# Optimization experiments

Measured on AMD Instinct MI355X. Metric: run time of the kernel, lower is better.

The kernel has to match this reference:

```python
import jax, jax.numpy as jnp
import numpy as np

N_NODES = 100000
N_EDGES = 1600000
IN_SIZE, HID_SIZE, OUT_SIZE = 128, 64, 64


def _glorot(key, shape):
    lim = float(np.sqrt(6.0 / (shape[0] + shape[1])))
    return jax.random.uniform(key, shape, jnp.float32, -lim, lim)


def setup_inputs() -> dict:
    key = jax.random.key(0)
    ks = jax.random.split(key, 6)
    features = jax.random.normal(ks[0], (N_NODES, IN_SIZE), jnp.float32)
    src = jax.random.randint(ks[1], (N_EDGES,), 0, N_NODES)
    dst = jax.random.randint(ks[2], (N_EDGES,), 0, N_NODES)
    return {
        "features": features,
        "W0": _glorot(ks[3], (IN_SIZE, HID_SIZE)),
        "b0": jnp.zeros((HID_SIZE,), jnp.float32),
        "W1": _glorot(ks[4], (HID_SIZE, HID_SIZE)),
        "b1": jnp.zeros((HID_SIZE,), jnp.float32),
        "W2": _glorot(ks[5], (HID_SIZE, OUT_SIZE)),
        "b2": jnp.zeros((OUT_SIZE,), jnp.float32),
        "src": src,
        "dst": dst,
    }


def reference(features, W0, b0, W1, b1, W2, b2, src, dst):
    # DGL GraphConv with norm='both': h' = relu(D_in^{-1/2} A D_out^{-1/2} h W + b)
    # Dropout layers are identity in eval mode (deterministic baseline).
    N = features.shape[0]
    ones = jnp.ones(src.shape, features.dtype)
    deg_out = jax.ops.segment_sum(ones, src, num_segments=N)
    deg_in = jax.ops.segment_sum(ones, dst, num_segments=N)
    norm_src = jnp.where(deg_out > 0, deg_out, 1.0) ** -0.5  # [N]
    norm_dst = jnp.where(deg_in > 0, deg_in, 1.0) ** -0.5    # [N]

    def layer(h, W, b):
        h = h * norm_src[:, None]          # source-side degree norm
        m = (h @ W)[src]                   # project first (in >= out), then gather [E, d_out]
        agg = jax.ops.segment_sum(m, dst, num_segments=N)  # scatter-add to destinations
        return jax.nn.relu(agg * norm_dst[:, None] + b)

    h = layer(features, W0, b0)
    h = layer(h, W1, b1)
    return layer(h, W2, b2)
```

## Files before the change

kernel.cpp:

```cpp
#include <hip/hip_runtime.h>
#include <hip/hip_bf16.h>

typedef __hip_bfloat16 bf16;
typedef __attribute__((ext_vector_type(8))) short bf16x8;
typedef __attribute__((ext_vector_type(8))) unsigned short u16x8;
typedef __attribute__((ext_vector_type(4))) float f32x4;
typedef __attribute__((ext_vector_type(4))) int i32x4;
typedef __attribute__((ext_vector_type(4))) short s16x4;

__device__ __forceinline__ float b2f(unsigned short u) {
  return __uint_as_float(((unsigned)u) << 16);
}
__device__ __forceinline__ unsigned short f2b(float x) {
  bf16 h = __float2bfloat16(x);
  return *reinterpret_cast<unsigned short*>(&h);
}

__global__ void k_passA(const int* __restrict__ src, const int* __restrict__ dst, int E,
                        int nbuck, int M, int* __restrict__ counts,
                        const unsigned short* __restrict__ raw, int* __restrict__ flag) {
  if (blockIdx.x == 256) {
    __shared__ int sbad, snz;
    const int t = threadIdx.x;
    if (t == 0) { sbad = 0; snz = 0; }
    __syncthreads();
    const unsigned short u = raw[t];
    const float a = fabsf(b2f(u));
    if (!(a < 100.f)) atomicAdd(&sbad, 1);
    if (((t & 1) == 0) && u != 0) atomicAdd(&snz, 1);
    __syncthreads();
    if (t == 0) flag[0] = (sbad == 0 && snz > 0) ? 1 : 0;
    return;
  }
  extern __shared__ int lh[];
  int* lh1 = lh;
  int* lh2 = lh + nbuck;
  const int t = threadIdx.x;
  for (int k = t; k < 2 * nbuck; k += 256) lh[k] = 0;
  __syncthreads();
  const int chunk = (E + 255) / 256;
  const int s = blockIdx.x * chunk;
  const int e = min(E, s + chunk);
  for (int i = s + t; i < e; i += 256) {
    atomicAdd(&lh1[dst[i] >> 8], 1);
    atomicAdd(&lh2[src[i] >> 8], 1);
  }
  __syncthreads();
  for (int k = t; k < nbuck; k += 256) {
    counts[k * 256 + blockIdx.x] = lh1[k];
    counts[M + k * 256 + blockIdx.x] = lh2[k];
  }
}

__global__ void k_scan1(const int* __restrict__ a, int M2, int* __restrict__ bsums) {
  __shared__ int sdata[256];
  int i = blockIdx.x * 256 + threadIdx.x;
  int v = (i < M2) ? a[i] : 0;
  sdata[threadIdx.x] = v;
  __syncthreads();
  for (int s = 128; s > 0; s >>= 1) {
    if (threadIdx.x < s) sdata[threadIdx.x] += sdata[threadIdx.x + s];
    __syncthreads();
  }
  if (threadIdx.x == 0) bsums[blockIdx.x] = sdata[0];
}

__global__ void k_scan2(int* __restrict__ bsums, int nb, int* __restrict__ rowStart,
                        int N, int E) {
  __shared__ int s[1024];
  const int t = threadIdx.x;
  const int v = (t < nb) ? bsums[t] : 0;
  s[t] = v;
  __syncthreads();
  for (int off = 1; off < 1024; off <<= 1) {
    int u = (t >= off) ? s[t - off] : 0;
    __syncthreads();
    s[t] += u;
    __syncthreads();
  }
  if (t < nb) bsums[t] = s[t] - v;
  if (t == 0) rowStart[N] = E;
}

__global__ void k_scan3(int* __restrict__ a, int M2, const int* __restrict__ bsums) {
  __shared__ int sdata[256];
  int i = blockIdx.x * 256 + threadIdx.x;
  int v = (i < M2) ? a[i] : 0;
  sdata[threadIdx.x] = v;
  __syncthreads();
  for (int off = 1; off < 256; off <<= 1) {
    int t = (threadIdx.x >= off) ? sdata[threadIdx.x - off] : 0;
    __syncthreads();
    sdata[threadIdx.x] += t;
    __syncthreads();
  }
  if (i < M2) a[i] = bsums[blockIdx.x] + sdata[threadIdx.x] - v;
}

__global__ void k_passC(const int* __restrict__ src, const int* __restrict__ dst, int E,
                        int nbuck, int M, const int* __restrict__ S,
                        int* __restrict__ tmp, unsigned char* __restrict__ tmp2) {
  extern __shared__ int cur[];
  int* cur1 = cur;
  int* cur2 = cur + nbuck;
  const int t = threadIdx.x;
  for (int k = t; k < nbuck; k += 256) {
    cur1[k] = S[k * 256 + blockIdx.x];
    cur2[k] = S[M + k * 256 + blockIdx.x];
  }
  __syncthreads();
  const int chunk = (E + 255) / 256;
  const int s = blockIdx.x * chunk;
  const int e = min(E, s + chunk);
  for (int i = s + t; i < e; i += 256) {
    const int sv = src[i];
    const int d = dst[i];
    const int pos1 = atomicAdd(&cur1[d >> 8], 1);
    tmp[pos1] = sv | ((d & 255) << 20);
    const int pos2 = atomicAdd(&cur2[sv >> 8], 1);
    tmp2[pos2 - E] = (unsigned char)(sv & 255);
  }
}

__global__ void k_passD(const int* __restrict__ tmp, const unsigned char* __restrict__ tmp2,
                        const int* __restrict__ S, int nbuck, int M, int N, int E,
                        int* __restrict__ rowStart, int* __restrict__ edgeSrc,
                        float* __restrict__ ns, float* __restrict__ nd) {
  __shared__ int h[256];
  __shared__ int ex[256];
  __shared__ int c[256];
  const int t = threadIdx.x;
  const int k = blockIdx.x;
  const int node = k * 256 + t;
  const int bs2 = S[M + k * 256] - E;
  const int be2 = (k + 1 < nbuck) ? (S[M + (k + 1) * 256] - E) : E;
  h[t] = 0;
  __syncthreads();
  for (int i = bs2 + t; i < be2; i += 256) atomicAdd(&h[tmp2[i]], 1);
  __syncthreads();
  if (node < N) {
    int dov = h[t];
    if (dov <= 0) dov = 1;
    ns[node] = rsqrtf((float)dov);
  }
  __syncthreads();
  const int bs = S[k * 256];
  const int be = (k + 1 < nbuck) ? S[(k + 1) * 256] : E;
  h[t] = 0;
  __syncthreads();
  for (int i = bs + t; i < be; i += 256) atomicAdd(&h[tmp[i] >> 20], 1);
  __syncthreads();
  const int cnt = h[t];
  ex[t] = cnt;
  __syncthreads();
  for (int off = 1; off < 256; off <<= 1) {
    int u = (t >= off) ? ex[t - off] : 0;
    __syncthreads();
    ex[t] += u;
    __syncthreads();
  }
  const int excl = ex[t] - cnt;
  if (node < N) {
    rowStart[node] = bs + excl;
    nd[node] = rsqrtf((float)(cnt > 0 ? cnt : 1));
  }
  c[t] = bs + excl;
  __syncthreads();
  for (int i = bs + t; i < be; i += 256) {
    const int v = tmp[i];
    const int pos = atomicAdd(&c[v >> 20], 1);
    edgeSrc[pos] = v & 0xFFFFF;
  }
}

__global__ void k_prepW(const void* __restrict__ W0, const void* __restrict__ W1,
                        const void* __restrict__ W2, const int* __restrict__ flag,
                        unsigned short* __restrict__ WT0, unsigned short* __restrict__ WT1,
                        unsigned short* __restrict__ WT2) {
  const bool isb = (*flag != 0);
  const int i = blockIdx.x * 256 + threadIdx.x;
  if (i < 8192) {
    const int n = i >> 7, k = i & 127;
    const float v = isb ? b2f(((const unsigned short*)W0)[k * 64 + n])
                        : ((const float*)W0)[k * 64 + n];
    WT0[i] = f2b(v);
  } else if (i < 12288) {
    const int j = i - 8192;
    const int n = j >> 6, k = j & 63;
    const float v = isb ? b2f(((const unsigned short*)W1)[k * 64 + n])
                        : ((const float*)W1)[k * 64 + n];
    WT1[j] = f2b(v);
  } else if (i < 16384) {
    const int j = i - 12288;
    const int n = j >> 6, k = j & 63;
    const float v = isb ? b2f(((const unsigned short*)W2)[k * 64 + n])
                        : ((const float*)W2)[k * 64 + n];
    WT2[j] = f2b(v);
  }
}

template <int K, bool FIRST, bool SCALE>
__device__ __forceinline__ void gemm_loadA(const void* hin, bool isb, int rowA,
                                           int quad, bf16x8* A) {
  constexpr int KT = K / 32;
  if (FIRST && !isb) {
    const float* hp = (const float*)hin + (size_t)rowA * K;
#pragma unroll
    for (int kt = 0; kt < KT; ++kt) {
      const float4 u0 = *(const float4*)(hp + kt * 32 + quad * 8);
      const float4 u1 = *(const float4*)(hp + kt * 32 + quad * 8 + 4);
      A[kt][0] = (short)f2b(u0.x); A[kt][1] = (short)f2b(u0.y);
      A[kt][2] = (short)f2b(u0.z); A[kt][3] = (short)f2b(u0.w);
      A[kt][4] = (short)f2b(u1.x); A[kt][5] = (short)f2b(u1.y);
      A[kt][6] = (short)f2b(u1.z); A[kt][7] = (short)f2b(u1.w);
    }
  } else {
    const unsigned short* hp = (const unsigned short*)hin + (size_t)rowA * K;
#pragma unroll
    for (int kt = 0; kt < KT; ++kt)
      A[kt] = *(const bf16x8*)(hp + kt * 32 + quad * 8);
  }
}

template <int K, bool FIRST, bool SCALE>
__global__ void __launch_bounds__(256) k_gemm(
    const void* __restrict__ hin, const unsigned short* __restrict__ WT,
    const int* __restrict__ flag, const float* __restrict__ norm_src,
    int N, unsigned short* __restrict__ out) {
  constexpr int KT = K / 32;
  constexpr int CST = 72;
  __shared__ unsigned short Cl[4][16 * CST];
  const bool isb = (*flag != 0);
  const int tid = threadIdx.x;
  const int lane = tid & 63;
  const int quad = lane >> 4;
  const int l16 = lane & 15;
  const int w = tid >> 6;
  unsigned short* myC = &Cl[w][0];

  bf16x8 Bf[KT][4];
#pragma unroll
  for (int kt = 0; kt < KT; ++kt)
#pragma unroll
    for (int nt = 0; nt < 4; ++nt)
      Bf[kt][nt] = *(const bf16x8*)(WT + (size_t)(nt * 16 + l16) * K + kt * 32 + quad * 8);

  const int wid = blockIdx.x * 4 + w;
  const int nw = gridDim.x * 4;
  const int G = (N + 15) >> 4;

  bf16x8 A0[KT], A1[KT];
  if (wid < G) {
    int r0 = (wid << 4) + l16;
    if (r0 >= N) r0 = N - 1;
    gemm_loadA<K, FIRST, SCALE>(hin, isb, r0, quad, A0);
  }
  for (int g = wid; g < G; g += nw) {
    if (g + nw < G) {
      int r1 = ((g + nw) << 4) + l16;
      if (r1 >= N) r1 = N - 1;
      gemm_loadA<K, FIRST, SCALE>(hin, isb, r1, quad, A1);
    }
    f32x4 acc[4] = {{0.f, 0.f, 0.f, 0.f}, {0.f, 0.f, 0.f, 0.f},
                    {0.f, 0.f, 0.f, 0.f}, {0.f, 0.f, 0.f, 0.f}};
#pragma unroll
    for (int kt = 0; kt < KT; ++kt) {
#pragma unroll
      for (int nt = 0; nt < 4; ++nt)
        acc[nt] = __builtin_amdgcn_mfma_f32_16x16x32_bf16(A0[kt], Bf[kt][nt], acc[nt], 0, 0, 0);
    }
    const int rowD = quad * 4;
#pragma unroll
    for (int r = 0; r < 4; ++r) {
      const int nodeW = (g << 4) + rowD + r;
      const float f = (SCALE && nodeW < N) ? norm_src[nodeW] : 1.0f;
#pragma unroll
      for (int nt = 0; nt < 4; ++nt)
        myC[(rowD + r) * CST + nt * 16 + l16] = f2b(SCALE ? acc[nt][r] * f : acc[nt][r]);
    }
    const int row2 = lane >> 2;
    const int c0 = (lane & 3) * 16;
    const int node = (g << 4) + row2;
    if (node < N) {
      const u16x8 v0 = *(const u16x8*)&myC[row2 * CST + c0];
      const u16x8 v1 = *(const u16x8*)&myC[row2 * CST + c0 + 8];
      *(u16x8*)(out + (size_t)node * 64 + c0) = v0;
      *(u16x8*)(out + (size_t)node * 64 + c0 + 8) = v1;
    }
#pragma unroll
    for (int kt = 0; kt < KT; ++kt) A0[kt] = A1[kt];
  }
}

__device__ __forceinline__ void agg_chunk_compute(unsigned trbase, int cb32, int lo,
                                                  unsigned span, int quad, f32x4* acc) {
  const int posbase = cb32 + (quad << 2);
  const unsigned u0 = (unsigned)(posbase - lo);
  bf16x8 Af;
#pragma unroll
  for (int j = 0; j < 8; ++j) {
    const unsigned off = (j < 4) ? (unsigned)j : (unsigned)(12 + j);
    Af[j] = ((u0 + off) < span) ? (short)0x3F80 : (short)0;
  }
  s16x4 t0[4], t1[4];
#pragma unroll
  for (int nt = 0; nt < 4; ++nt) {
    const unsigned a = trbase + (unsigned)(nt * 1024);
    asm volatile("ds_read_b64_tr_b16 %0, %1" : "=v"(t0[nt]) : "v"(a) : "memory");
    asm volatile("ds_read_b64_tr_b16 %0, %1 offset:512" : "=v"(t1[nt]) : "v"(a) : "memory");
  }
  asm volatile("s_waitcnt lgkmcnt(0)" ::: "memory");
  __builtin_amdgcn_sched_barrier(0);
#pragma unroll
  for (int nt = 0; nt < 4; ++nt) {
    bf16x8 Bf;
    Bf[0] = t0[nt][0]; Bf[1] = t0[nt][1]; Bf[2] = t0[nt][2]; Bf[3] = t0[nt][3];
    Bf[4] = t1[nt][0]; Bf[5] = t1[nt][1]; Bf[6] = t1[nt][2]; Bf[7] = t1[nt][3];
    acc[nt] = __builtin_amdgcn_mfma_f32_16x16x32_bf16(Af, Bf, acc[nt], 0, 0, 0);
  }
}

template <bool LAST>
__global__ void __launch_bounds__(256) k_aggregate(
    const unsigned short* __restrict__ proj,
    const int* __restrict__ edgeSrc, const int* __restrict__ rowStart,
    const float* __restrict__ norm_dst, const float* __restrict__ norm_src,
    const void* __restrict__ bias, const int* __restrict__ flag,
    int N, int E, void* __restrict__ outp) {
  __shared__ unsigned short lds[4][2048];
  const bool isb = (*flag != 0);
  const int tid = threadIdx.x;
  const int w = tid >> 6;
  const int lane = tid & 63;
  const int l16 = lane & 15;
  const int quad = lane >> 4;
  const int e32 = lane & 31;
  const int p = lane >> 5;

  const int wid = blockIdx.x * 4 + w;
  const int g0 = wid * 8;

  float bcol[4];
#pragma unroll
  for (int nt = 0; nt < 4; ++nt) {
    const int col = nt * 16 + l16;
    bcol[nt] = isb ? b2f(((const unsigned short*)bias)[col]) : ((const float*)bias)[col];
  }

  const int cb = rowStart[min(g0, N)];
  const int ce = rowStart[min(g0 + 8, N)];
  const int L = ce - cb;
  const int nch = (L + 31) >> 5;

  const int rsi = min(g0 + min(l16, 8), N);
  const int rsj = min(g0 + min(l16 + 1, 8), N);
  const int lo = rowStart[rsi];
  const unsigned span = (unsigned)(rowStart[rsj] - lo);

  int idxc[6];
#pragma unroll
  for (int t = 0; t < 6; ++t) {
    const int pos = min(cb + t * 32 + e32, E - 1);
    idxc[t] = edgeSrc[pos];
  }

  unsigned short* myl = &lds[w][0];
  unsigned wofs[4];
#pragma unroll
  for (int q = 0; q < 4; ++q) {
    const int n0 = p * 32 + q * 8;
    wofs[q] = (unsigned)((n0 >> 4) * 512 + e32 * 16 + (n0 & 15));
  }
  const unsigned trbase = (unsigned)(uintptr_t)myl + (unsigned)lane * 8u;

  f32x4 acc[4] = {{0.f, 0.f, 0.f, 0.f}, {0.f, 0.f, 0.f, 0.f},
                  {0.f, 0.f, 0.f, 0.f}, {0.f, 0.f, 0.f, 0.f}};

  i32x4 gb[4][4];
#define AGG_ISSUE(t, b)                                                         \
  {                                                                             \
    const unsigned short* rp = proj + (size_t)idxc[t] * 64 + p * 32;            \
    gb[b][0] = *(const i32x4*)(rp);                                             \
    gb[b][1] = *(const i32x4*)(rp + 8);                                         \
    gb[b][2] = *(const i32x4*)(rp + 16);                                        \
    gb[b][3] = *(const i32x4*)(rp + 24);                                        \
  }
  if (0 < nch) AGG_ISSUE(0, 0);
  if (1 < nch) AGG_ISSUE(1, 1);
  if (2 < nch) AGG_ISSUE(2, 2);
  if (3 < nch) AGG_ISSUE(3, 3);

#pragma unroll
  for (int tt = 0; tt < 6; ++tt) {
    if (tt < nch) {
#pragma unroll
      for (int q = 0; q < 4; ++q) *(i32x4*)(myl + wofs[q]) = gb[tt & 3][q];
      if (tt + 4 < 6 && tt + 4 < nch) AGG_ISSUE(tt + 4, tt & 3);
      asm volatile("s_waitcnt lgkmcnt(0)" ::: "memory");
      agg_chunk_compute(trbase, cb + tt * 32, lo, span, quad, acc);
    }
  }
  for (int t = 6; t < nch; ++t) {
    const int pos = min(cb + t * 32 + e32, E - 1);
    const int idx = edgeSrc[pos];
    const unsigned short* rp = proj + (size_t)idx * 64 + p * 32;
    i32x4 g4[4];
    g4[0] = *(const i32x4*)(rp);
    g4[1] = *(const i32x4*)(rp + 8);
    g4[2] = *(const i32x4*)(rp + 16);
    g4[3] = *(const i32x4*)(rp + 24);
#pragma unroll
    for (int q = 0; q < 4; ++q) *(i32x4*)(myl + wofs[q]) = g4[q];
    asm volatile("s_waitcnt lgkmcnt(0)" ::: "memory");
    agg_chunk_compute(trbase, cb + t * 32, lo, span, quad, acc);
  }
#undef AGG_ISSUE

  if (LAST && !isb) {
    float* fs = (float*)myl;
#pragma unroll
    for (int reg = 0; reg < 4; ++reg) {
      const int row = quad * 4 + reg;
      if (row < 8) {
        const int node = min(g0 + row, N - 1);
        const float nd = norm_dst[node];
#pragma unroll
        for (int nt = 0; nt < 4; ++nt)
          fs[row * 64 + nt * 16 + l16] = fmaxf(fmaf(acc[nt][reg], nd, bcol[nt]), 0.f);
      }
    }
    asm volatile("s_waitcnt lgkmcnt(0)" ::: "memory");
    __builtin_amdgcn_sched_barrier(0);
    const int r = lane >> 3;
    const int c0 = (lane & 7) * 8;
    const int node = g0 + r;
    if (node < N) {
      const float4 v0 = *(const float4*)&fs[r * 64 + c0];
      const float4 v1 = *(const float4*)&fs[r * 64 + c0 + 4];
      float* of = (float*)outp + (size_t)node * 64 + c0;
      *(float4*)of = v0;
      *(float4*)(of + 4) = v1;
    }
  } else {
#pragma unroll
    for (int reg = 0; reg < 4; ++reg) {
      const int row = quad * 4 + reg;
      if (row < 8) {
        const int node = min(g0 + row, N - 1);
        const float nd = norm_dst[node];
        const float esc = LAST ? 1.f : norm_src[node];
#pragma unroll
        for (int nt = 0; nt < 4; ++nt) {
          float x = fmaxf(fmaf(acc[nt][reg], nd, bcol[nt]), 0.f);
          if (!LAST) x *= esc;
          myl[row * 64 + nt * 16 + l16] = f2b(x);
        }
      }
    }
    asm volatile("s_waitcnt lgkmcnt(0)" ::: "memory");
    __builtin_amdgcn_sched_barrier(0);
    if (lane < 32) {
      const int r = lane >> 2;
      const int c0 = (lane & 3) * 16;
      const int node = g0 + r;
      if (node < N) {
        const u16x8 v0 = *(const u16x8*)&myl[r * 64 + c0];
        const u16x8 v1 = *(const u16x8*)&myl[r * 64 + c0 + 8];
        *(u16x8*)((unsigned short*)outp + (size_t)node * 64 + c0) = v0;
        *(u16x8*)((unsigned short*)outp + (size_t)node * 64 + c0 + 8) = v1;
      }
    }
  }
}

extern "C" void kernel_launch(void* const* d_in, const int* in_sizes, int n_in,
                              void* d_out, int out_size, void* d_ws, size_t ws_size,
                              hipStream_t stream) {
  const void* features = d_in[0];
  const void* W0 = d_in[1];
  const void* b0 = d_in[2];
  const void* W1 = d_in[3];
  const void* b1 = d_in[4];
  const void* W2 = d_in[5];
  const void* b2 = d_in[6];
  const int* src = (const int*)d_in[7];
  const int* dst = (const int*)d_in[8];
  const int N = in_sizes[0] / 128;
  const int E = in_sizes[7];
  const int NBUCK = (N + 255) >> 8;
  const int M = NBUCK * 256;
  const int M2 = 2 * M;

  char* w = (char*)d_ws;
  size_t off = 0;
  auto alloc = [&](size_t bytes) {
    void* p = w + off;
    off = (off + bytes + 255) & ~(size_t)255;
    return p;
  };
  int* flag = (int*)alloc(4);
  int* rowStart = (int*)alloc((size_t)(N + 1) * 4);
  int* counts = (int*)alloc((size_t)M2 * 4);
  int* bsums = (int*)alloc(1024 * 4);
  float* norm_src = (float*)alloc((size_t)N * 4);
  float* norm_dst = (float*)alloc((size_t)N * 4);
  int* tmp = (int*)alloc((size_t)E * 4);
  unsigned char* tmp2 = (unsigned char*)alloc((size_t)E);
  int* edgeSrc = (int*)alloc((size_t)E * 4);
  unsigned short* projA = (unsigned short*)alloc((size_t)N * 64 * 2);
  unsigned short* WT0 = (unsigned short*)alloc(64 * 128 * 2);
  unsigned short* WT1 = (unsigned short*)alloc(64 * 64 * 2);
  unsigned short* WT2 = (unsigned short*)alloc(64 * 64 * 2);
  unsigned short* hB = (unsigned short*)d_out;

  const size_t lds_nb = (size_t)NBUCK * 2 * 4;
  const int G16 = (N + 15) / 16;
  const int GB = (G16 + 7) / 8;

  k_passA<<<257, 256, lds_nb, stream>>>(src, dst, E, NBUCK, M, counts,
                                        (const unsigned short*)features, flag);
  const int NB2 = (M2 + 255) / 256;
  k_scan1<<<NB2, 256, 0, stream>>>(counts, M2, bsums);
  k_scan2<<<1, 1024, 0, stream>>>(bsums, NB2, rowStart, N, E);
  k_scan3<<<NB2, 256, 0, stream>>>(counts, M2, bsums);
  k_passC<<<256, 256, lds_nb, stream>>>(src, dst, E, NBUCK, M, counts, tmp, tmp2);
  k_passD<<<NBUCK, 256, 0, stream>>>(tmp, tmp2, counts, NBUCK, M, N, E,
                                     rowStart, edgeSrc, norm_src, norm_dst);
  k_prepW<<<64, 256, 0, stream>>>(W0, W1, W2, flag, WT0, WT1, WT2);

  const int AB = (((N + 7) / 8) + 3) / 4;
  k_gemm<128, true, true><<<GB, 256, 0, stream>>>(features, WT0, flag, norm_src, N, projA);
  k_aggregate<false><<<AB, 256, 0, stream>>>(projA, edgeSrc, rowStart, norm_dst, norm_src, b0, flag, N, E, hB);
  k_gemm<64, false, false><<<GB, 256, 0, stream>>>(hB, WT1, flag, nullptr, N, projA);
  k_aggregate<false><<<AB, 256, 0, stream>>>(projA, edgeSrc, rowStart, norm_dst, norm_src, b1, flag, N, E, hB);
  k_gemm<64, false, false><<<GB, 256, 0, stream>>>(hB, WT2, flag, nullptr, N, projA);
  k_aggregate<true><<<AB, 256, 0, stream>>>(projA, edgeSrc, rowStart, norm_dst, norm_src, b2, flag, N, E, d_out);
}
```

Baseline: 335.3 us.

## Use global atomic out-degree, fold weight prep into GEMM, shrink gather prefetch

Out-degree is now counted with global atomics into a memset array rather than through a second bucket histogram, scatter and per-bucket count. This removes the tmp2 byte array, halves the scan size and drops work from passC and passD. The separate weight-transpose kernel is gone: each GEMM block converts and transposes its weight matrix into LDS and reads B fragments from there. The aggregation prefetch depth is reduced from 4 to 2 chunks. The trade-offs are contended global atomics on random source ids, redundant per-block weight loading, and less latency hiding in the gather.

```diff
diff --git a/kernel.cpp b/kernel.cpp
--- a/kernel.cpp
+++ b/kernel.cpp
@@ -17,8 +17,9 @@
 }
 
 __global__ void k_passA(const int* __restrict__ src, const int* __restrict__ dst, int E,
-                        int nbuck, int M, int* __restrict__ counts,
-                        const unsigned short* __restrict__ raw, int* __restrict__ flag) {
+                        int nbuck, int* __restrict__ counts,
+                        const unsigned short* __restrict__ raw, int* __restrict__ flag,
+                        int* __restrict__ degout) {
   if (blockIdx.x == 256) {
     __shared__ int sbad, snz;
     const int t = threadIdx.x;
@@ -32,30 +33,25 @@
     if (t == 0) flag[0] = (sbad == 0 && snz > 0) ? 1 : 0;
     return;
   }
-  extern __shared__ int lh[];
-  int* lh1 = lh;
-  int* lh2 = lh + nbuck;
+  extern __shared__ int lh1[];
   const int t = threadIdx.x;
-  for (int k = t; k < 2 * nbuck; k += 256) lh[k] = 0;
+  for (int k = t; k < nbuck; k += 256) lh1[k] = 0;
   __syncthreads();
   const int chunk = (E + 255) / 256;
   const int s = blockIdx.x * chunk;
   const int e = min(E, s + chunk);
   for (int i = s + t; i < e; i += 256) {
     atomicAdd(&lh1[dst[i] >> 8], 1);
-    atomicAdd(&lh2[src[i] >> 8], 1);
-  }
-  __syncthreads();
-  for (int k = t; k < nbuck; k += 256) {
-    counts[k * 256 + blockIdx.x] = lh1[k];
-    counts[M + k * 256 + blockIdx.x] = lh2[k];
-  }
-}
-
-__global__ void k_scan1(const int* __restrict__ a, int M2, int* __restrict__ bsums) {
+    atomicAdd(&degout[src[i]], 1);
+  }
+  __syncthreads();
+  for (int k = t; k < nbuck; k += 256) counts[k * 256 + blockIdx.x] = lh1[k];
+}
+
+__global__ void k_scan1(const int* __restrict__ a, int M, int* __restrict__ bsums) {
   __shared__ int sdata[256];
   int i = blockIdx.x * 256 + threadIdx.x;
-  int v = (i < M2) ? a[i] : 0;
+  int v = (i < M) ? a[i] : 0;
   sdata[threadIdx.x] = v;
   __syncthreads();
   for (int s = 128; s > 0; s >>= 1) {
@@ -82,10 +78,10 @@
   if (t == 0) rowStart[N] = E;
 }
 
-__global__ void k_scan3(int* __restrict__ a, int M2, const int* __restrict__ bsums) {
+__global__ void k_scan3(int* __restrict__ a, int M, const int* __restrict__ bsums) {
   __shared__ int sdata[256];
   int i = blockIdx.x * 256 + threadIdx.x;
-  int v = (i < M2) ? a[i] : 0;
+  int v = (i < M) ? a[i] : 0;
   sdata[threadIdx.x] = v;
   __syncthreads();
   for (int off = 1; off < 256; off <<= 1) {
@@ -94,20 +90,14 @@
     sdata[threadIdx.x] += t;
     __syncthreads();
   }
-  if (i < M2) a[i] = bsums[blockIdx.x] + sdata[threadIdx.x] - v;
+  if (i < M) a[i] = bsums[blockIdx.x] + sdata[threadIdx.x] - v;
 }
 
 __global__ void k_passC(const int* __restrict__ src, const int* __restrict__ dst, int E,
-                        int nbuck, int M, const int* __restrict__ S,
-                        int* __restrict__ tmp, unsigned char* __restrict__ tmp2) {
-  extern __shared__ int cur[];
-  int* cur1 = cur;
-  int* cur2 = cur + nbuck;
+                        int nbuck, const int* __restrict__ S, int* __restrict__ tmp) {
+  extern __shared__ int cur1[];
   const int t = threadIdx.x;
-  for (int k = t; k < nbuck; k += 256) {
-    cur1[k] = S[k * 256 + blockIdx.x];
-    cur2[k] = S[M + k * 256 + blockIdx.x];
-  }
+  for (int k = t; k < nbuck; k += 256) cur1[k] = S[k * 256 + blockIdx.x];
   __syncthreads();
   const int chunk = (E + 255) / 256;
   const int s = blockIdx.x * chunk;
@@ -117,14 +107,13 @@
     const int d = dst[i];
     const int pos1 = atomicAdd(&cur1[d >> 8], 1);
     tmp[pos1] = sv | ((d & 255) << 20);
-    const int pos2 = atomicAdd(&cur2[sv >> 8], 1);
-    tmp2[pos2 - E] = (unsigned char)(sv & 255);
-  }
-}
-
-__global__ void k_passD(const int* __restrict__ tmp, const unsigned char* __restrict__ tmp2,
-                        const int* __restrict__ S, int nbuck, int M, int N, int E,
+  }
+}
+
+__global__ void k_passD(const int* __restrict__ tmp, const int* __restrict__ S,
+                        int nbuck, int N, int E,
                         int* __restrict__ rowStart, int* __restrict__ edgeSrc,
+                        const int* __restrict__ degout,
                         float* __restrict__ ns, float* __restrict__ nd) {
   __shared__ int h[256];
   __shared__ int ex[256];
@@ -132,18 +121,6 @@
   const int t = threadIdx.x;
   const int k = blockIdx.x;
   const int node = k * 256 + t;
-  const int bs2 = S[M + k * 256] - E;
-  const int be2 = (k + 1 < nbuck) ? (S[M + (k + 1) * 256] - E) : E;
-  h[t] = 0;
-  __syncthreads();
-  for (int i = bs2 + t; i < be2; i += 256) atomicAdd(&h[tmp2[i]], 1);
-  __syncthreads();
-  if (node < N) {
-    int dov = h[t];
-    if (dov <= 0) dov = 1;
-    ns[node] = rsqrtf((float)dov);
-  }
-  __syncthreads();
   const int bs = S[k * 256];
   const int be = (k + 1 < nbuck) ? S[(k + 1) * 256] : E;
   h[t] = 0;
@@ -163,6 +140,9 @@
   if (node < N) {
     rowStart[node] = bs + excl;
     nd[node] = rsqrtf((float)(cnt > 0 ? cnt : 1));
+    int dov = degout[node];
+    if (dov <= 0) dov = 1;
+    ns[node] = rsqrtf((float)dov);
   }
   c[t] = bs + excl;
   __syncthreads();
@@ -170,32 +150,6 @@
     const int v = tmp[i];
     const int pos = atomicAdd(&c[v >> 20], 1);
     edgeSrc[pos] = v & 0xFFFFF;
-  }
-}
-
-__global__ void k_prepW(const void* __restrict__ W0, const void* __restrict__ W1,
-                        const void* __restrict__ W2, const int* __restrict__ flag,
-                        unsigned short* __restrict__ WT0, unsigned short* __restrict__ WT1,
-                        unsigned short* __restrict__ WT2) {
-  const bool isb = (*flag != 0);
-  const int i = blockIdx.x * 256 + threadIdx.x;
-  if (i < 8192) {
-    const int n = i >> 7, k = i & 127;
-    const float v = isb ? b2f(((const unsigned short*)W0)[k * 64 + n])
-                        : ((const float*)W0)[k * 64 + n];
-    WT0[i] = f2b(v);
-  } else if (i < 12288) {
-    const int j = i - 8192;
-    const int n = j >> 6, k = j & 63;
-    const float v = isb ? b2f(((const unsigned short*)W1)[k * 64 + n])
-                        : ((const float*)W1)[k * 64 + n];
-    WT1[j] = f2b(v);
-  } else if (i < 16384) {
-    const int j = i - 12288;
-    const int n = j >> 6, k = j & 63;
-    const float v = isb ? b2f(((const unsigned short*)W2)[k * 64 + n])
-                        : ((const float*)W2)[k * 64 + n];
-    WT2[j] = f2b(v);
   }
 }
 
@@ -224,27 +178,46 @@
 
 template <int K, bool FIRST, bool SCALE>
 __global__ void __launch_bounds__(256) k_gemm(
-    const void* __restrict__ hin, const unsigned short* __restrict__ WT,
+    const void* __restrict__ hin, const void* __restrict__ Wv,
     const int* __restrict__ flag, const float* __restrict__ norm_src,
     int N, unsigned short* __restrict__ out) {
   constexpr int KT = K / 32;
+  constexpr int ST = K + 8;
   constexpr int CST = 72;
+  __shared__ unsigned short Wl[64 * ST];
   __shared__ unsigned short Cl[4][16 * CST];
   const bool isb = (*flag != 0);
   const int tid = threadIdx.x;
+
+  {
+    const unsigned short* Wus = (const unsigned short*)Wv;
+    const float* Wf = (const float*)Wv;
+    for (int i0 = tid * 8; i0 < K * 64; i0 += 2048) {
+      const int k = i0 >> 6;
+      const int n0 = i0 & 63;
+      unsigned short v[8];
+      if (isb) {
+        const u16x8 u = *(const u16x8*)(Wus + i0);
+#pragma unroll
+        for (int j = 0; j < 8; ++j) v[j] = u[j];
+      } else {
+        const float4 f0 = *(const float4*)(Wf + i0);
+        const float4 f1 = *(const float4*)(Wf + i0 + 4);
+        v[0] = f2b(f0.x); v[1] = f2b(f0.y); v[2] = f2b(f0.z); v[3] = f2b(f0.w);
+        v[4] = f2b(f1.x); v[5] = f2b(f1.y); v[6] = f2b(f1.z); v[7] = f2b(f1.w);
+      }
+#pragma unroll
+      for (int j = 0; j < 8; ++j) Wl[(n0 + j) * ST + k] = v[j];
+    }
+  }
+  __syncthreads();
+
   const int lane = tid & 63;
   const int quad = lane >> 4;
   const int l16 = lane & 15;
   const int w = tid >> 6;
   unsigned short* myC = &Cl[w][0];
 
-  bf16x8 Bf[KT][4];
-#pragma unroll
-  for (int kt = 0; kt < KT; ++kt)
-#pragma unroll
-    for (int nt = 0; nt < 4; ++nt)
-      Bf[kt][nt] = *(const bf16x8*)(WT + (size_t)(nt * 16 + l16) * K + kt * 32 + quad * 8);
-
   const int wid = blockIdx.x * 4 + w;
   const int nw = gridDim.x * 4;
   const int G = (N + 15) >> 4;
@@ -265,9 +238,12 @@
                     {0.f, 0.f, 0.f, 0.f}, {0.f, 0.f, 0.f, 0.f}};
 #pragma unroll
     for (int kt = 0; kt < KT; ++kt) {
-#pragma unroll
-      for (int nt = 0; nt < 4; ++nt)
-        acc[nt] = __builtin_amdgcn_mfma_f32_16x16x32_bf16(A0[kt], Bf[kt][nt], acc[nt], 0, 0, 0);
+      const int koff = kt * 32 + quad * 8;
+#pragma unroll
+      for (int nt = 0; nt < 4; ++nt) {
+        const bf16x8 Bf = *(const bf16x8*)&Wl[(nt * 16 + l16) * ST + koff];
+        acc[nt] = __builtin_amdgcn_mfma_f32_16x16x32_bf16(A0[kt], Bf, acc[nt], 0, 0, 0);
+      }
     }
     const int rowD = quad * 4;
 #pragma unroll
@@ -376,7 +352,7 @@
   f32x4 acc[4] = {{0.f, 0.f, 0.f, 0.f}, {0.f, 0.f, 0.f, 0.f},
                   {0.f, 0.f, 0.f, 0.f}, {0.f, 0.f, 0.f, 0.f}};
 
-  i32x4 gb[4][4];
+  i32x4 gb[2][4];
 #define AGG_ISSUE(t, b)                                                         \
   {                                                                             \
     const unsigned short* rp = proj + (size_t)idxc[t] * 64 + p * 32;            \
@@ -387,15 +363,13 @@
   }
   if (0 < nch) AGG_ISSUE(0, 0);
   if (1 < nch) AGG_ISSUE(1, 1);
-  if (2 < nch) AGG_ISSUE(2, 2);
-  if (3 < nch) AGG_ISSUE(3, 3);
 
 #pragma unroll
   for (int tt = 0; tt < 6; ++tt) {
     if (tt < nch) {
 #pragma unroll
-      for (int q = 0; q < 4; ++q) *(i32x4*)(myl + wofs[q]) = gb[tt & 3][q];
-      if (tt + 4 < 6 && tt + 4 < nch) AGG_ISSUE(tt + 4, tt & 3);
+      for (int q = 0; q < 4; ++q) *(i32x4*)(myl + wofs[q]) = gb[tt & 1][q];
+      if (tt + 2 < 6 && tt + 2 < nch) AGG_ISSUE(tt + 2, tt & 1);
       asm volatile("s_waitcnt lgkmcnt(0)" ::: "memory");
       agg_chunk_compute(trbase, cb + tt * 32, lo, span, quad, acc);
     }
@@ -489,7 +463,6 @@
   const int E = in_sizes[7];
   const int NBUCK = (N + 255) >> 8;
   const int M = NBUCK * 256;
-  const int M2 = 2 * M;
 
   char* w = (char*)d_ws;
   size_t off = 0;
@@ -500,39 +473,35 @@
   };
   int* flag = (int*)alloc(4);
   int* rowStart = (int*)alloc((size_t)(N + 1) * 4);
-  int* counts = (int*)alloc((size_t)M2 * 4);
+  int* counts = (int*)alloc((size_t)M * 4);
   int* bsums = (int*)alloc(1024 * 4);
   float* norm_src = (float*)alloc((size_t)N * 4);
   float* norm_dst = (float*)alloc((size_t)N * 4);
+  int* degout = (int*)alloc((size_t)N * 4);
   int* tmp = (int*)alloc((size_t)E * 4);
-  unsigned char* tmp2 = (unsigned char*)alloc((size_t)E);
   int* edgeSrc = (int*)alloc((size_t)E * 4);
   unsigned short* projA = (unsigned short*)alloc((size_t)N * 64 * 2);
-  unsigned short* WT0 = (unsigned short*)alloc(64 * 128 * 2);
-  unsigned short* WT1 = (unsigned short*)alloc(64 * 64 * 2);
-  unsigned short* WT2 = (unsigned short*)alloc(64 * 64 * 2);
   unsigned short* hB = (unsigned short*)d_out;
 
-  const size_t lds_nb = (size_t)NBUCK * 2 * 4;
+  const size_t lds_nb = (size_t)NBUCK * 4;
   const int G16 = (N + 15) / 16;
   const int GB = (G16 + 7) / 8;
 
-  k_passA<<<257, 256, lds_nb, stream>>>(src, dst, E, NBUCK, M, counts,
-                                        (const unsigned short*)features, flag);
-  const int NB2 = (M2 + 255) / 256;
-  k_scan1<<<NB2, 256, 0, stream>>>(counts, M2, bsums);
-  k_scan2<<<1, 1024, 0, stream>>>(bsums, NB2, rowStart, N, E);
-  k_scan3<<<NB2, 256, 0, stream>>>(counts, M2, bsums);
-  k_passC<<<256, 256, lds_nb, stream>>>(src, dst, E, NBUCK, M, counts, tmp, tmp2);
-  k_passD<<<NBUCK, 256, 0, stream>>>(tmp, tmp2, counts, NBUCK, M, N, E,
-                                     rowStart, edgeSrc, norm_src, norm_dst);
-  k_prepW<<<64, 256, 0, stream>>>(W0, W1, W2, flag, WT0, WT1, WT2);
+  hipMemsetAsync(degout, 0, (size_t)N * 4, stream);
+  k_passA<<<257, 256, lds_nb, stream>>>(src, dst, E, NBUCK, counts,
+                                        (const unsigned short*)features, flag, degout);
+  k_scan1<<<NBUCK, 256, 0, stream>>>(counts, M, bsums);
+  k_scan2<<<1, 1024, 0, stream>>>(bsums, NBUCK, rowStart, N, E);
+  k_scan3<<<NBUCK, 256, 0, stream>>>(counts, M, bsums);
+  k_passC<<<256, 256, lds_nb, stream>>>(src, dst, E, NBUCK, counts, tmp);
+  k_passD<<<NBUCK, 256, 0, stream>>>(tmp, counts, NBUCK, N, E,
+                                     rowStart, edgeSrc, degout, norm_src, norm_dst);
 
   const int AB = (((N + 7) / 8) + 3) / 4;
-  k_gemm<128, true, true><<<GB, 256, 0, stream>>>(features, WT0, flag, norm_src, N, projA);
+  k_gemm<128, true, true><<<GB, 256, 0, stream>>>(features, W0, flag, norm_src, N, projA);
   k_aggregate<false><<<AB, 256, 0, stream>>>(projA, edgeSrc, rowStart, norm_dst, norm_src, b0, flag, N, E, hB);
-  k_gemm<64, false, false><<<GB, 256, 0, stream>>>(hB, WT1, flag, nullptr, N, projA);
+  k_gemm<64, false, false><<<GB, 256, 0, stream>>>(hB, W1, flag, nullptr, N, projA);
   k_aggregate<false><<<AB, 256, 0, stream>>>(projA, edgeSrc, rowStart, norm_dst, norm_src, b1, flag, N, E, hB);
-  k_gemm<64, false, false><<<GB, 256, 0, stream>>>(hB, WT2, flag, nullptr, N, projA);
+  k_gemm<64, false, false><<<GB, 256, 0, stream>>>(hB, W2, flag, nullptr, N, projA);
   k_aggregate<true><<<AB, 256, 0, stream>>>(projA, edgeSrc, rowStart, norm_dst, norm_src, b2, flag, N, E, d_out);
 }
```

Result: slower. 357.4 us (+6.6%).
